# Kernel optimization log

Measured on AMD Instinct MI355X. Metric: run time of the kernel, lower is better.

Reference implementation:

```python
import jax, jax.numpy as jnp
import numpy as np

N = 50000      # num_nodes
F_IN = 128     # num_features
E = 800000     # num edges (before self-loops)
H1, D1 = 8, 16 # conv1: 8 heads x 16 dims -> 128 concat
D2 = 8         # conv2: 1 head x 8 dims
NEG_SLOPE = 0.2


def setup_inputs() -> dict:
    key = jax.random.key(0)
    ks = jax.random.split(key, 16)
    s = 0.05
    return {
        "x": jax.random.normal(ks[0], (N, F_IN), jnp.float32),
        "edge_index": jax.random.randint(ks[1], (2, E), 0, N, dtype=jnp.int64),
        "W1": jax.random.normal(ks[2], (F_IN, H1 * D1), jnp.float32) * s,
        "att_src1": jax.random.normal(ks[3], (H1, D1), jnp.float32) * s,
        "att_dst1": jax.random.normal(ks[4], (H1, D1), jnp.float32) * s,
        "b1": jnp.zeros((H1 * D1,), jnp.float32),
        "W2": jax.random.normal(ks[5], (H1 * D1, D2), jnp.float32) * s,
        "att_src2": jax.random.normal(ks[6], (1, D2), jnp.float32) * s,
        "att_dst2": jax.random.normal(ks[7], (1, D2), jnp.float32) * s,
        "b2": jnp.zeros((D2,), jnp.float32),
        "fc1_w": jax.random.normal(ks[8], (N * D2, 84), jnp.float32) * 0.005,
        "fc1_b": jnp.zeros((84,), jnp.float32),
        "fc2_w": jax.random.normal(ks[9], (84, 24), jnp.float32) * s,
        "fc2_b": jnp.zeros((24,), jnp.float32),
        "fc3_w": jax.random.normal(ks[10], (24, 2), jnp.float32) * s,
        "fc3_b": jnp.zeros((2,), jnp.float32),
    }


def gat_conv(x, src, dst, W, att_src, att_dst, bias, heads, out_dim):
    """PyG GATConv: per-head linear, edge attention, scatter-softmax over
    incoming edges per target node, weighted scatter-add aggregation."""
    n = x.shape[0]
    h = (x @ W).reshape(n, heads, out_dim)            # [N,H,D]
    a_src = jnp.einsum('nhd,hd->nh', h, att_src)      # [N,H]
    a_dst = jnp.einsum('nhd,hd->nh', h, att_dst)      # [N,H]
    e = jax.nn.leaky_relu(a_src[src] + a_dst[dst], NEG_SLOPE)  # [Et,H]
    # softmax over edges grouped by destination node (stable)
    m = jax.ops.segment_max(e, dst, num_segments=n)
    p = jnp.exp(e - m[dst])
    denom = jax.ops.segment_sum(p, dst, num_segments=n)
    alpha = p / denom[dst]                            # [Et,H]
    out = jax.ops.segment_sum(alpha[:, :, None] * h[src], dst, num_segments=n)
    return out.reshape(n, heads * out_dim) + bias


def reference(x, edge_index, W1, att_src1, att_dst1, b1,
              W2, att_src2, att_dst2, b2,
              fc1_w, fc1_b, fc2_w, fc2_b, fc3_w, fc3_b):
    # add self-loops (GATConv default add_self_loops=True)
    loop = jnp.arange(N, dtype=edge_index.dtype)
    src = jnp.concatenate([edge_index[0], loop])
    dst = jnp.concatenate([edge_index[1], loop])

    h = jax.nn.elu(gat_conv(x, src, dst, W1, att_src1, att_dst1, b1, H1, D1))
    h = jax.nn.elu(gat_conv(h, src, dst, W2, att_src2, att_dst2, b2, 1, D2))

    z = h.reshape(1, N * D2)                          # batch of one graph
    z = jax.nn.elu(z @ fc1_w + fc1_b)
    z = jax.nn.elu(z @ fc2_w + fc2_b)
    z = z @ fc3_w + fc3_b
    return jax.nn.log_softmax(z, axis=1)              # [1,2]
```

## Files before the change

### kernel.cpp

```cpp
#include <hip/hip_runtime.h>
#include <math.h>

#define N_NODES 50000
#define F_IN 128
#define NE 800000
#define NH1 8
#define ND1 16
#define ND2 8
#define NEG 0.2f
#define ZLEN (N_NODES * ND2)

typedef __attribute__((ext_vector_type(8))) short bf16x8;
typedef __attribute__((ext_vector_type(4))) float f32x4;

__device__ __forceinline__ float lrelu(float v) { return v > 0.f ? v : NEG * v; }
__device__ __forceinline__ float elu1(float v)  { return v > 0.f ? v : (__expf(v) - 1.f); }

__device__ __forceinline__ unsigned short f2bf(float f) {
    union { float f; unsigned int i; } c; c.f = f;
    unsigned int u = c.i;
    return (unsigned short)((u + 0x7FFFu + ((u >> 16) & 1u)) >> 16);
}
__device__ __forceinline__ float bflo(unsigned int u) {
    union { unsigned int i; float f; } c; c.i = u << 16; return c.f;
}
__device__ __forceinline__ float bfhi(unsigned int u) {
    union { unsigned int i; float f; } c; c.i = u & 0xFFFF0000u; return c.f;
}
__device__ __forceinline__ int ei_is64(const int* __restrict__ ei) {
    return ((ei[1] | ei[3] | ei[5] | ei[7]) == 0) ? 1 : 0;
}

__global__ void init_counts_kernel(int* __restrict__ counts) {
    int i = blockIdx.x * blockDim.x + threadIdx.x;
    if (i < N_NODES) counts[i] = 1;
}

__global__ void hist_kernel(const int* __restrict__ ei, int* __restrict__ counts) {
    int e = blockIdx.x * blockDim.x + threadIdx.x;
    if (e >= NE) return;
    int is64 = ei_is64(ei);
    int d = is64 ? ei[2 * NE + 2 * e] : ei[NE + e];
    atomicAdd(&counts[d], 1);
}

__global__ __launch_bounds__(1024) void scan_kernel(const int* __restrict__ counts,
                                                    int* __restrict__ rowptr,
                                                    int* __restrict__ cursor) {
    __shared__ int wsum[16];
    __shared__ int wpre[16];
    __shared__ int s_total;
    const int t = threadIdx.x;
    const int lane = t & 63, w = t >> 6;
    int carry = 0;
    if (t == 0) rowptr[0] = 0;
    for (int base = 0; base < N_NODES; base += 1024) {
        int i = base + t;
        int orig = (i < N_NODES) ? counts[i] : 0;
        int v = orig;
        #pragma unroll
        for (int off = 1; off < 64; off <<= 1) {
            int u = __shfl_up(v, off, 64);
            if (lane >= off) v += u;
        }
        if (lane == 63) wsum[w] = v;
        __syncthreads();
        if (t == 0) {
            int s = 0;
            #pragma unroll
            for (int j = 0; j < 16; ++j) { wpre[j] = s; s += wsum[j]; }
            s_total = s;
        }
        __syncthreads();
        int incl = v + wpre[w] + carry;
        if (i < N_NODES) { rowptr[i + 1] = incl; cursor[i] = incl - orig; }
        carry += s_total;
        __syncthreads();
    }
}

__global__ void fill_kernel(const int* __restrict__ ei,
                            int* __restrict__ cursor, int* __restrict__ esrc) {
    int i = blockIdx.x * blockDim.x + threadIdx.x;
    if (i >= NE + N_NODES) return;
    int s, d;
    if (i < NE) {
        int is64 = ei_is64(ei);
        if (is64) { s = ei[2 * i]; d = ei[2 * NE + 2 * i]; }
        else      { s = ei[i];     d = ei[NE + i]; }
    } else {
        s = d = i - NE;
    }
    int slot = atomicAdd(&cursor[d], 1);
    esrc[slot] = s;
}

__global__ __launch_bounds__(256) void wprep_kernel(const float* __restrict__ W,
                                                    uint4* __restrict__ wbf) {
    int tid = blockIdx.x * 256 + threadIdx.x;
    int col = tid >> 4, kc = tid & 15;
    unsigned int u[4];
    #pragma unroll
    for (int jj = 0; jj < 4; ++jj) {
        unsigned int lo = f2bf(W[(kc * 8 + 2 * jj) * 128 + col]);
        unsigned int hi = f2bf(W[(kc * 8 + 2 * jj + 1) * 128 + col]);
        u[jj] = lo | (hi << 16);
    }
    uint4 v; v.x = u[0]; v.y = u[1]; v.z = u[2]; v.w = u[3];
    wbf[col * 16 + (kc ^ (col & 15))] = v;
}

__global__ __launch_bounds__(256) void gemm1_kernel(const float* __restrict__ x,
                                                    const uint4* __restrict__ wbf,
                                                    const float* __restrict__ att_src,
                                                    const float* __restrict__ att_dst,
                                                    unsigned int* __restrict__ h1b,
                                                    float* __restrict__ a_src1,
                                                    float* __restrict__ a_dst1) {
    __shared__ uint4 Xs[1024];
    __shared__ uint4 Ws[2048];
    const int t = threadIdx.x;
    const int row0 = blockIdx.x * 64;

    #pragma unroll
    for (int p = 0; p < 8; ++p) Ws[p * 256 + t] = wbf[p * 256 + t];

    #pragma unroll
    for (int p = 0; p < 4; ++p) {
        int cidx = p * 256 + t;
        int row = cidx >> 4, c = cidx & 15;
        int grow = row0 + row;
        float4 xa = make_float4(0.f, 0.f, 0.f, 0.f);
        float4 xb = make_float4(0.f, 0.f, 0.f, 0.f);
        if (grow < N_NODES) {
            xa = *reinterpret_cast<const float4*>(x + (size_t)grow * F_IN + c * 8);
            xb = *reinterpret_cast<const float4*>(x + (size_t)grow * F_IN + c * 8 + 4);
        }
        uint4 u;
        u.x = (unsigned int)f2bf(xa.x) | ((unsigned int)f2bf(xa.y) << 16);
        u.y = (unsigned int)f2bf(xa.z) | ((unsigned int)f2bf(xa.w) << 16);
        u.z = (unsigned int)f2bf(xb.x) | ((unsigned int)f2bf(xb.y) << 16);
        u.w = (unsigned int)f2bf(xb.z) | ((unsigned int)f2bf(xb.w) << 16);
        Xs[row * 16 + (c ^ (row & 15))] = u;
    }
    __syncthreads();

    const int wv = t >> 6;
    const int l  = t & 63;
    const int d  = l & 15;
    const int g  = l >> 4;
    const int arow = wv * 16 + d;

    f32x4 acc[8];
    #pragma unroll
    for (int n = 0; n < 8; ++n) { acc[n][0] = 0.f; acc[n][1] = 0.f; acc[n][2] = 0.f; acc[n][3] = 0.f; }

    #pragma unroll
    for (int ks = 0; ks < 4; ++ks) {
        int kc = ks * 4 + g;
        union { uint4 u; bf16x8 v; } A;
        A.u = Xs[arow * 16 + (kc ^ d)];
        #pragma unroll
        for (int n = 0; n < 8; ++n) {
            union { uint4 u; bf16x8 v; } B;
            B.u = Ws[(n * 16 + d) * 16 + (kc ^ d)];
            acc[n] = __builtin_amdgcn_mfma_f32_16x16x32_bf16(A.v, B.v, acc[n], 0, 0, 0);
        }
    }

    float as8[8], ad8[8];
    #pragma unroll
    for (int n = 0; n < 8; ++n) { as8[n] = att_src[n * 16 + d]; ad8[n] = att_dst[n * 16 + d]; }
    #pragma unroll
    for (int n = 0; n < 8; ++n) {
        #pragma unroll
        for (int r = 0; r < 4; ++r) {
            float ps = acc[n][r] * as8[n];
            float pd = acc[n][r] * ad8[n];
            #pragma unroll
            for (int off = 1; off < 16; off <<= 1) {
                ps += __shfl_xor(ps, off, 16);
                pd += __shfl_xor(pd, off, 16);
            }
            int grow = row0 + wv * 16 + g * 4 + r;
            if (d == 0 && grow < N_NODES) {
                a_src1[grow * 8 + n] = ps;
                a_dst1[grow * 8 + n] = pd;
            }
        }
    }
    #pragma unroll
    for (int n = 0; n < 8; ++n) {
        #pragma unroll
        for (int r = 0; r < 4; ++r) {
            float lo = acc[n][r];
            float hi = __shfl_xor(lo, 1, 64);
            int grow = row0 + wv * 16 + g * 4 + r;
            if (((d & 1) == 0) && grow < N_NODES) {
                unsigned int u = (unsigned int)f2bf(lo) | ((unsigned int)f2bf(hi) << 16);
                h1b[(size_t)grow * 64 + n * 8 + (d >> 1)] = u;
            }
        }
    }
}

__global__ __launch_bounds__(256) void agg1_kernel(const unsigned int* __restrict__ h1b,
                                                   const float* __restrict__ a_src,
                                                   const float* __restrict__ a_dst,
                                                   const int* __restrict__ rowptr,
                                                   const int* __restrict__ esrc,
                                                   const float* __restrict__ b1,
                                                   float* __restrict__ hout) {
    int wid = (blockIdx.x * 256 + threadIdx.x) >> 6;
    if (wid >= N_NODES) return;
    const int lane = threadIdx.x & 63;
    const int h = lane >> 3;
    const float ad = a_dst[wid * 8 + h];
    float acc0 = 0.f, acc1 = 0.f, den = 0.f;
    int j = rowptr[wid];
    const int jend = rowptr[wid + 1];
    for (; j + 4 <= jend; j += 4) {
        int s0 = esrc[j], s1 = esrc[j + 1], s2 = esrc[j + 2], s3 = esrc[j + 3];
        float e0 = a_src[s0 * 8 + h], e1 = a_src[s1 * 8 + h];
        float e2 = a_src[s2 * 8 + h], e3 = a_src[s3 * 8 + h];
        unsigned int u0 = h1b[(size_t)s0 * 64 + lane];
        unsigned int u1 = h1b[(size_t)s1 * 64 + lane];
        unsigned int u2 = h1b[(size_t)s2 * 64 + lane];
        unsigned int u3 = h1b[(size_t)s3 * 64 + lane];
        float p0 = __expf(lrelu(e0 + ad));
        float p1 = __expf(lrelu(e1 + ad));
        float p2 = __expf(lrelu(e2 + ad));
        float p3 = __expf(lrelu(e3 + ad));
        den += (p0 + p1) + (p2 + p3);
        acc0 = fmaf(p0, bflo(u0), acc0); acc1 = fmaf(p0, bfhi(u0), acc1);
        acc0 = fmaf(p1, bflo(u1), acc0); acc1 = fmaf(p1, bfhi(u1), acc1);
        acc0 = fmaf(p2, bflo(u2), acc0); acc1 = fmaf(p2, bfhi(u2), acc1);
        acc0 = fmaf(p3, bflo(u3), acc0); acc1 = fmaf(p3, bfhi(u3), acc1);
    }
    for (; j < jend; ++j) {
        int s = esrc[j];
        float e = a_src[s * 8 + h];
        unsigned int u = h1b[(size_t)s * 64 + lane];
        float p = __expf(lrelu(e + ad));
        den += p;
        acc0 = fmaf(p, bflo(u), acc0);
        acc1 = fmaf(p, bfhi(u), acc1);
    }
    float inv = 1.f / den;
    float2 bb = *reinterpret_cast<const float2*>(b1 + 2 * lane);
    float o0 = elu1(acc0 * inv + bb.x);
    float o1 = elu1(acc1 * inv + bb.y);
    *reinterpret_cast<float2*>(hout + (size_t)wid * F_IN + 2 * lane) = make_float2(o0, o1);
}

__global__ __launch_bounds__(256) void gemm2_kernel(const float* __restrict__ h,
                                                    const float* __restrict__ W2,
                                                    const float* __restrict__ att_src2,
                                                    const float* __restrict__ att_dst2,
                                                    float* __restrict__ h2,
                                                    float* __restrict__ a_src2,
                                                    float* __restrict__ a_dst2) {
    __shared__ float Ws[F_IN * ND2];
    __shared__ float Hs[32 * 132];
    int t = threadIdx.x;
    int node0 = blockIdx.x * 32;
    #pragma unroll
    for (int i = 0; i < 4; ++i) { int idx = i * 256 + t; Ws[idx] = W2[idx]; }
    #pragma unroll
    for (int i = 0; i < 4; ++i) {
        int fidx = i * 256 + t;
        int r = fidx >> 5;
        int c4 = fidx & 31;
        int grow = node0 + r;
        float4 v = make_float4(0.f, 0.f, 0.f, 0.f);
        if (grow < N_NODES) v = *reinterpret_cast<const float4*>(h + (size_t)grow * F_IN + c4 * 4);
        *reinterpret_cast<float4*>(&Hs[r * 132 + c4 * 4]) = v;
    }
    __syncthreads();
    int nsub = t >> 3, d = t & 7;
    int node = node0 + nsub;
    float acc = 0.f;
    #pragma unroll 8
    for (int k = 0; k < F_IN; ++k)
        acc = fmaf(Hs[nsub * 132 + k], Ws[k * ND2 + d], acc);
    float vs = acc * att_src2[d];
    float vd = acc * att_dst2[d];
    #pragma unroll
    for (int off = 4; off >= 1; off >>= 1) {
        vs += __shfl_xor(vs, off, 8);
        vd += __shfl_xor(vd, off, 8);
    }
    if (node < N_NODES) {
        h2[node * ND2 + d] = acc;
        if (d == 0) { a_src2[node] = vs; a_dst2[node] = vd; }
    }
}

__global__ __launch_bounds__(256) void agg2fc1_kernel(const float* __restrict__ h2,
                                                      const float* __restrict__ a_src2,
                                                      const float* __restrict__ a_dst2,
                                                      const int* __restrict__ rowptr,
                                                      const int* __restrict__ esrc,
                                                      const float* __restrict__ b2,
                                                      const float* __restrict__ w,
                                                      float* __restrict__ partial) {
    __shared__ float zs[2048];
    __shared__ float4 red[252];
    const int t = threadIdx.x;
    const int n = blockIdx.x * 256 + t;

    float z[8] = {0.f, 0.f, 0.f, 0.f, 0.f, 0.f, 0.f, 0.f};
    if (n < N_NODES) {
        float ad = a_dst2[n];
        float den = 0.f;
        const int jend = rowptr[n + 1];
        for (int j = rowptr[n]; j < jend; ++j) {
            int s = esrc[j];
            float p = __expf(lrelu(a_src2[s] + ad));
            den += p;
            float4 va = *reinterpret_cast<const float4*>(h2 + s * ND2);
            float4 vb = *reinterpret_cast<const float4*>(h2 + s * ND2 + 4);
            z[0] = fmaf(p, va.x, z[0]); z[1] = fmaf(p, va.y, z[1]);
            z[2] = fmaf(p, va.z, z[2]); z[3] = fmaf(p, va.w, z[3]);
            z[4] = fmaf(p, vb.x, z[4]); z[5] = fmaf(p, vb.y, z[5]);
            z[6] = fmaf(p, vb.z, z[6]); z[7] = fmaf(p, vb.w, z[7]);
        }
        float inv = 1.f / den;
        #pragma unroll
        for (int k = 0; k < 8; ++k) z[k] = elu1(z[k] * inv + b2[k]);
    }
    *reinterpret_cast<float4*>(&zs[t * 8])     = make_float4(z[0], z[1], z[2], z[3]);
    *reinterpret_cast<float4*>(&zs[t * 8 + 4]) = make_float4(z[4], z[5], z[6], z[7]);
    __syncthreads();

    const int c4 = t % 21;
    const int rr = t / 21;
    if (t < 252) {
        float4 a = make_float4(0.f, 0.f, 0.f, 0.f);
        const float4* __restrict__ w4 = reinterpret_cast<const float4*>(w);
        const size_t R0 = (size_t)blockIdx.x * 2048;
        if (R0 + 2048 <= (size_t)ZLEN) {
            for (int gq = 0; gq < 34; ++gq) {
                float4 wv[5];
                float  zv[5];
                #pragma unroll
                for (int u = 0; u < 5; ++u) {
                    int i = (gq * 5 + u) * 12 + rr;
                    wv[u] = w4[(R0 + i) * 21 + c4];
                    zv[u] = zs[i];
                }
                #pragma unroll
                for (int u = 0; u < 5; ++u) {
                    a.x = fmaf(zv[u], wv[u].x, a.x);
                    a.y = fmaf(zv[u], wv[u].y, a.y);
                    a.z = fmaf(zv[u], wv[u].z, a.z);
                    a.w = fmaf(zv[u], wv[u].w, a.w);
                }
            }
            if (rr < 8) {
                int i = 2040 + rr;
                float4 wv = w4[(R0 + i) * 21 + c4];
                float  zv = zs[i];
                a.x = fmaf(zv, wv.x, a.x); a.y = fmaf(zv, wv.y, a.y);
                a.z = fmaf(zv, wv.z, a.z); a.w = fmaf(zv, wv.w, a.w);
            }
        } else {
            for (int i = rr; i < 2048; i += 12) {
                if (R0 + i < (size_t)ZLEN) {
                    float4 wv = w4[(R0 + i) * 21 + c4];
                    float  zv = zs[i];
                    a.x = fmaf(zv, wv.x, a.x); a.y = fmaf(zv, wv.y, a.y);
                    a.z = fmaf(zv, wv.z, a.z); a.w = fmaf(zv, wv.w, a.w);
                }
            }
        }
        red[t] = a;
    }
    __syncthreads();
    if (t < 21) {
        float4 s = red[t];
        #pragma unroll
        for (int k = 1; k < 12; ++k) {
            float4 v = red[k * 21 + t];
            s.x += v.x; s.y += v.y; s.z += v.z; s.w += v.w;
        }
        *reinterpret_cast<float4*>(partial + (size_t)blockIdx.x * 88 + t * 4) = s;
    }
}

__global__ __launch_bounds__(256) void fctail_kernel(const float* __restrict__ partial,
                                                     const float* __restrict__ fc1_b,
                                                     const float* __restrict__ fc2_w,
                                                     const float* __restrict__ fc2_b,
                                                     const float* __restrict__ fc3_w,
                                                     const float* __restrict__ fc3_b,
                                                     float* __restrict__ out) {
    __shared__ float red[252];
    __shared__ float z1[84];
    __shared__ float z2[24];
    const int t = threadIdx.x;
    if (t < 252) {
        const int j = t % 84;
        const int sl = t / 84;
        const int b0 = sl * 66;
        const int b1 = (b0 + 66 < 196) ? (b0 + 66) : 196;
        float s = 0.f;
        for (int b = b0; b < b1; b += 2)
            s += partial[(size_t)b * 88 + j] + partial[(size_t)(b + 1) * 88 + j];
        red[t] = s;
    }
    __syncthreads();
    if (t < 84) z1[t] = elu1(red[t] + red[t + 84] + red[t + 168] + fc1_b[t]);
    __syncthreads();
    if (t < 24) {
        float a = fc2_b[t];
        for (int i = 0; i < 84; ++i) a = fmaf(z1[i], fc2_w[i * 24 + t], a);
        z2[t] = elu1(a);
    }
    __syncthreads();
    if (t == 0) {
        float z3[2];
        #pragma unroll
        for (int jj = 0; jj < 2; ++jj) {
            float a = fc3_b[jj];
            for (int i = 0; i < 24; ++i) a = fmaf(z2[i], fc3_w[i * 2 + jj], a);
            z3[jj] = a;
        }
        float m = fmaxf(z3[0], z3[1]);
        float l = m + logf(__expf(z3[0] - m) + __expf(z3[1] - m));
        out[0] = z3[0] - l;
        out[1] = z3[1] - l;
    }
}

extern "C" void kernel_launch(void* const* d_in, const int* in_sizes, int n_in,
                              void* d_out, int out_size, void* d_ws, size_t ws_size,
                              hipStream_t stream) {
    const float* x        = (const float*)d_in[0];
    const int*   ei       = (const int*)d_in[1];
    const float* W1       = (const float*)d_in[2];
    const float* att_src1 = (const float*)d_in[3];
    const float* att_dst1 = (const float*)d_in[4];
    const float* b1       = (const float*)d_in[5];
    const float* W2       = (const float*)d_in[6];
    const float* att_src2 = (const float*)d_in[7];
    const float* att_dst2 = (const float*)d_in[8];
    const float* b2       = (const float*)d_in[9];
    const float* fc1_w    = (const float*)d_in[10];
    const float* fc1_b    = (const float*)d_in[11];
    const float* fc2_w    = (const float*)d_in[12];
    const float* fc2_b    = (const float*)d_in[13];
    const float* fc3_w    = (const float*)d_in[14];
    const float* fc3_b    = (const float*)d_in[15];
    float* out = (float*)d_out;

    char* ws = (char*)d_ws;
    unsigned int* h1b = (unsigned int*)(ws + 0);
    float* hbuf   = (float*)(ws + 12800000);
    float* a_src1 = (float*)(ws + 38400000);
    float* a_dst1 = (float*)(ws + 40000000);
    float* h2     = (float*)(ws + 41600000);
    float* a_src2 = (float*)(ws + 43200000);
    float* a_dst2 = (float*)(ws + 43400000);
    int*   counts = (int*)  (ws + 43600000);
    int*   rowptr = (int*)  (ws + 43800000);
    int*   cursor = (int*)  (ws + 44000064);
    int*   esrc   = (int*)  (ws + 44200064);
    float* partial= (float*)(ws + 47600064);
    uint4* wbf    = (uint4*)(ws + 47669056);

    wprep_kernel<<<8, 256, 0, stream>>>(W1, wbf);
    init_counts_kernel<<<(N_NODES + 255) / 256, 256, 0, stream>>>(counts);
    hist_kernel<<<(NE + 255) / 256, 256, 0, stream>>>(ei, counts);
    scan_kernel<<<1, 1024, 0, stream>>>(counts, rowptr, cursor);
    fill_kernel<<<(NE + N_NODES + 255) / 256, 256, 0, stream>>>(ei, cursor, esrc);

    gemm1_kernel<<<(N_NODES + 63) / 64, 256, 0, stream>>>(x, wbf, att_src1, att_dst1, h1b, a_src1, a_dst1);
    agg1_kernel<<<(N_NODES + 3) / 4, 256, 0, stream>>>(h1b, a_src1, a_dst1, rowptr, esrc, b1, hbuf);

    gemm2_kernel<<<(N_NODES + 31) / 32, 256, 0, stream>>>(hbuf, W2, att_src2, att_dst2, h2, a_src2, a_dst2);
    agg2fc1_kernel<<<(N_NODES + 255) / 256, 256, 0, stream>>>(h2, a_src2, a_dst2, rowptr, esrc, b2, fc1_w, partial);
    fctail_kernel<<<1, 256, 0, stream>>>(partial, fc1_b, fc2_w, fc2_b, fc3_w, fc3_b, out);
}
```

Measured before the change: 273.9 us.

## Parallelize scan, split agg2 from FC1, widen FC1 grid, unroll agg1 by eight

The single-block serial scan is replaced by a three-kernel multi-block scan. The fused agg2+fc1 kernel is split into a standalone agg2 kernel that writes node features to a buffer, followed by an fc1 stage launched with many more blocks (240 rows each), so streaming the 134MB fc1 weight uses the whole GPU rather than 196 blocks. wprep and init_counts are merged into one prep kernel, and agg1 gains an 8-wide unrolled gather loop for more memory-level parallelism. The cost is extra launches, an intermediate buffer round trip and a larger final reduction over partial sums.

```diff
diff --git a/kernel.cpp b/kernel.cpp
--- a/kernel.cpp
+++ b/kernel.cpp
@@ -9,6 +9,9 @@
 #define ND2 8
 #define NEG 0.2f
 #define ZLEN (N_NODES * ND2)
+#define NBLK 196
+#define FC1_RPB 240
+#define FC1_NB 1667
 
 typedef __attribute__((ext_vector_type(8))) short bf16x8;
 typedef __attribute__((ext_vector_type(4))) float f32x4;
@@ -31,9 +34,23 @@
     return ((ei[1] | ei[3] | ei[5] | ei[7]) == 0) ? 1 : 0;
 }
 
-__global__ void init_counts_kernel(int* __restrict__ counts) {
-    int i = blockIdx.x * blockDim.x + threadIdx.x;
+__global__ __launch_bounds__(256) void prep_kernel(const float* __restrict__ W,
+                                                   uint4* __restrict__ wbf,
+                                                   int* __restrict__ counts) {
+    int i = blockIdx.x * 256 + threadIdx.x;
     if (i < N_NODES) counts[i] = 1;
+    if (i < 2048) {
+        int col = i >> 4, kc = i & 15;
+        unsigned int u[4];
+        #pragma unroll
+        for (int jj = 0; jj < 4; ++jj) {
+            unsigned int lo = f2bf(W[(kc * 8 + 2 * jj) * 128 + col]);
+            unsigned int hi = f2bf(W[(kc * 8 + 2 * jj + 1) * 128 + col]);
+            u[jj] = lo | (hi << 16);
+        }
+        uint4 v; v.x = u[0]; v.y = u[1]; v.z = u[2]; v.w = u[3];
+        wbf[col * 16 + (kc ^ (col & 15))] = v;
+    }
 }
 
 __global__ void hist_kernel(const int* __restrict__ ei, int* __restrict__ counts) {
@@ -44,39 +61,62 @@
     atomicAdd(&counts[d], 1);
 }
 
-__global__ __launch_bounds__(1024) void scan_kernel(const int* __restrict__ counts,
+__global__ __launch_bounds__(256) void scan1_kernel(const int* __restrict__ counts,
+                                                    int* __restrict__ bsum) {
+    const int t = threadIdx.x;
+    int i = blockIdx.x * 256 + t;
+    int v = (i < N_NODES) ? counts[i] : 0;
+    #pragma unroll
+    for (int off = 32; off; off >>= 1) v += __shfl_down(v, off, 64);
+    __shared__ int ws[4];
+    if ((t & 63) == 0) ws[t >> 6] = v;
+    __syncthreads();
+    if (t == 0) bsum[blockIdx.x] = ws[0] + ws[1] + ws[2] + ws[3];
+}
+
+__global__ __launch_bounds__(256) void scan2_kernel(const int* __restrict__ bsum,
+                                                    int* __restrict__ boff) {
+    const int t = threadIdx.x;
+    const int lane = t & 63, w = t >> 6;
+    int v = (t < NBLK) ? bsum[t] : 0;
+    int incl = v;
+    #pragma unroll
+    for (int off = 1; off < 64; off <<= 1) {
+        int u = __shfl_up(incl, off, 64);
+        if (lane >= off) incl += u;
+    }
+    __shared__ int wsum[4];
+    __shared__ int wpre[4];
+    if (lane == 63) wsum[w] = incl;
+    __syncthreads();
+    if (t == 0) { int s = 0; for (int j = 0; j < 4; ++j) { wpre[j] = s; s += wsum[j]; } }
+    __syncthreads();
+    if (t < NBLK) boff[t] = incl - v + wpre[w];
+}
+
+__global__ __launch_bounds__(256) void scan3_kernel(const int* __restrict__ counts,
+                                                    const int* __restrict__ boff,
                                                     int* __restrict__ rowptr,
                                                     int* __restrict__ cursor) {
-    __shared__ int wsum[16];
-    __shared__ int wpre[16];
-    __shared__ int s_total;
     const int t = threadIdx.x;
     const int lane = t & 63, w = t >> 6;
-    int carry = 0;
-    if (t == 0) rowptr[0] = 0;
-    for (int base = 0; base < N_NODES; base += 1024) {
-        int i = base + t;
-        int orig = (i < N_NODES) ? counts[i] : 0;
-        int v = orig;
-        #pragma unroll
-        for (int off = 1; off < 64; off <<= 1) {
-            int u = __shfl_up(v, off, 64);
-            if (lane >= off) v += u;
-        }
-        if (lane == 63) wsum[w] = v;
-        __syncthreads();
-        if (t == 0) {
-            int s = 0;
-            #pragma unroll
-            for (int j = 0; j < 16; ++j) { wpre[j] = s; s += wsum[j]; }
-            s_total = s;
-        }
-        __syncthreads();
-        int incl = v + wpre[w] + carry;
-        if (i < N_NODES) { rowptr[i + 1] = incl; cursor[i] = incl - orig; }
-        carry += s_total;
-        __syncthreads();
-    }
+    int i = blockIdx.x * 256 + t;
+    int v = (i < N_NODES) ? counts[i] : 0;
+    int incl = v;
+    #pragma unroll
+    for (int off = 1; off < 64; off <<= 1) {
+        int u = __shfl_up(incl, off, 64);
+        if (lane >= off) incl += u;
+    }
+    __shared__ int wsum[4];
+    __shared__ int wpre[4];
+    if (lane == 63) wsum[w] = incl;
+    __syncthreads();
+    if (t == 0) { int s = 0; for (int j = 0; j < 4; ++j) { wpre[j] = s; s += wsum[j]; } }
+    __syncthreads();
+    incl += wpre[w] + boff[blockIdx.x];
+    if (i < N_NODES) { rowptr[i + 1] = incl; cursor[i] = incl - v; }
+    if (i == 0) rowptr[0] = 0;
 }
 
 __global__ void fill_kernel(const int* __restrict__ ei,
@@ -93,21 +133,6 @@
     }
     int slot = atomicAdd(&cursor[d], 1);
     esrc[slot] = s;
-}
-
-__global__ __launch_bounds__(256) void wprep_kernel(const float* __restrict__ W,
-                                                    uint4* __restrict__ wbf) {
-    int tid = blockIdx.x * 256 + threadIdx.x;
-    int col = tid >> 4, kc = tid & 15;
-    unsigned int u[4];
-    #pragma unroll
-    for (int jj = 0; jj < 4; ++jj) {
-        unsigned int lo = f2bf(W[(kc * 8 + 2 * jj) * 128 + col]);
-        unsigned int hi = f2bf(W[(kc * 8 + 2 * jj + 1) * 128 + col]);
-        u[jj] = lo | (hi << 16);
-    }
-    uint4 v; v.x = u[0]; v.y = u[1]; v.z = u[2]; v.w = u[3];
-    wbf[col * 16 + (kc ^ (col & 15))] = v;
 }
 
 __global__ __launch_bounds__(256) void gemm1_kernel(const float* __restrict__ x,
@@ -219,14 +244,32 @@
     float acc0 = 0.f, acc1 = 0.f, den = 0.f;
     int j = rowptr[wid];
     const int jend = rowptr[wid + 1];
+    for (; j + 8 <= jend; j += 8) {
+        int s[8];
+        #pragma unroll
+        for (int k = 0; k < 8; ++k) s[k] = esrc[j + k];
+        unsigned int u[8];
+        #pragma unroll
+        for (int k = 0; k < 8; ++k) u[k] = h1b[(size_t)s[k] * 64 + lane];
+        float e[8];
+        #pragma unroll
+        for (int k = 0; k < 8; ++k) e[k] = a_src[s[k] * 8 + h];
+        #pragma unroll
+        for (int k = 0; k < 8; ++k) {
+            float p = __expf(lrelu(e[k] + ad));
+            den += p;
+            acc0 = fmaf(p, bflo(u[k]), acc0);
+            acc1 = fmaf(p, bfhi(u[k]), acc1);
+        }
+    }
     for (; j + 4 <= jend; j += 4) {
         int s0 = esrc[j], s1 = esrc[j + 1], s2 = esrc[j + 2], s3 = esrc[j + 3];
-        float e0 = a_src[s0 * 8 + h], e1 = a_src[s1 * 8 + h];
-        float e2 = a_src[s2 * 8 + h], e3 = a_src[s3 * 8 + h];
         unsigned int u0 = h1b[(size_t)s0 * 64 + lane];
         unsigned int u1 = h1b[(size_t)s1 * 64 + lane];
         unsigned int u2 = h1b[(size_t)s2 * 64 + lane];
         unsigned int u3 = h1b[(size_t)s3 * 64 + lane];
+        float e0 = a_src[s0 * 8 + h], e1 = a_src[s1 * 8 + h];
+        float e2 = a_src[s2 * 8 + h], e3 = a_src[s3 * 8 + h];
         float p0 = __expf(lrelu(e0 + ad));
         float p1 = __expf(lrelu(e1 + ad));
         float p2 = __expf(lrelu(e2 + ad));
@@ -239,8 +282,8 @@
     }
     for (; j < jend; ++j) {
         int s = esrc[j];
+        unsigned int u = h1b[(size_t)s * 64 + lane];
         float e = a_src[s * 8 + h];
-        unsigned int u = h1b[(size_t)s * 64 + lane];
         float p = __expf(lrelu(e + ad));
         den += p;
         acc0 = fmaf(p, bflo(u), acc0);
@@ -296,78 +339,77 @@
     }
 }
 
-__global__ __launch_bounds__(256) void agg2fc1_kernel(const float* __restrict__ h2,
-                                                      const float* __restrict__ a_src2,
-                                                      const float* __restrict__ a_dst2,
-                                                      const int* __restrict__ rowptr,
-                                                      const int* __restrict__ esrc,
-                                                      const float* __restrict__ b2,
-                                                      const float* __restrict__ w,
-                                                      float* __restrict__ partial) {
-    __shared__ float zs[2048];
+__global__ void agg2_kernel(const float* __restrict__ h2,
+                            const float* __restrict__ a_src2, const float* __restrict__ a_dst2,
+                            const int* __restrict__ rowptr, const int* __restrict__ esrc,
+                            const float* __restrict__ b2, float* __restrict__ g) {
+    int n = blockIdx.x * blockDim.x + threadIdx.x;
+    if (n >= N_NODES) return;
+    float ad = a_dst2[n];
+    float acc[8] = {0.f, 0.f, 0.f, 0.f, 0.f, 0.f, 0.f, 0.f};
+    float den = 0.f;
+    int jend = rowptr[n + 1];
+    for (int j = rowptr[n]; j < jend; ++j) {
+        int s = esrc[j];
+        float p = __expf(lrelu(a_src2[s] + ad));
+        den += p;
+        float4 va = *reinterpret_cast<const float4*>(h2 + s * ND2);
+        float4 vb = *reinterpret_cast<const float4*>(h2 + s * ND2 + 4);
+        acc[0] = fmaf(p, va.x, acc[0]); acc[1] = fmaf(p, va.y, acc[1]);
+        acc[2] = fmaf(p, va.z, acc[2]); acc[3] = fmaf(p, va.w, acc[3]);
+        acc[4] = fmaf(p, vb.x, acc[4]); acc[5] = fmaf(p, vb.y, acc[5]);
+        acc[6] = fmaf(p, vb.z, acc[6]); acc[7] = fmaf(p, vb.w, acc[7]);
+    }
+    float inv = 1.f / den;
+    float4 o0 = make_float4(elu1(acc[0] * inv + b2[0]), elu1(acc[1] * inv + b2[1]),
+                            elu1(acc[2] * inv + b2[2]), elu1(acc[3] * inv + b2[3]));
+    float4 o1 = make_float4(elu1(acc[4] * inv + b2[4]), elu1(acc[5] * inv + b2[5]),
+                            elu1(acc[6] * inv + b2[6]), elu1(acc[7] * inv + b2[7]));
+    *reinterpret_cast<float4*>(g + n * ND2)     = o0;
+    *reinterpret_cast<float4*>(g + n * ND2 + 4) = o1;
+}
+
+__global__ __launch_bounds__(256) void fc1_stage1(const float* __restrict__ z,
+                                                  const float* __restrict__ w,
+                                                  float* __restrict__ partial) {
+    __shared__ float zs[FC1_RPB];
     __shared__ float4 red[252];
     const int t = threadIdx.x;
-    const int n = blockIdx.x * 256 + t;
-
-    float z[8] = {0.f, 0.f, 0.f, 0.f, 0.f, 0.f, 0.f, 0.f};
-    if (n < N_NODES) {
-        float ad = a_dst2[n];
-        float den = 0.f;
-        const int jend = rowptr[n + 1];
-        for (int j = rowptr[n]; j < jend; ++j) {
-            int s = esrc[j];
-            float p = __expf(lrelu(a_src2[s] + ad));
-            den += p;
-            float4 va = *reinterpret_cast<const float4*>(h2 + s * ND2);
-            float4 vb = *reinterpret_cast<const float4*>(h2 + s * ND2 + 4);
-            z[0] = fmaf(p, va.x, z[0]); z[1] = fmaf(p, va.y, z[1]);
-            z[2] = fmaf(p, va.z, z[2]); z[3] = fmaf(p, va.w, z[3]);
-            z[4] = fmaf(p, vb.x, z[4]); z[5] = fmaf(p, vb.y, z[5]);
-            z[6] = fmaf(p, vb.z, z[6]); z[7] = fmaf(p, vb.w, z[7]);
-        }
-        float inv = 1.f / den;
-        #pragma unroll
-        for (int k = 0; k < 8; ++k) z[k] = elu1(z[k] * inv + b2[k]);
-    }
-    *reinterpret_cast<float4*>(&zs[t * 8])     = make_float4(z[0], z[1], z[2], z[3]);
-    *reinterpret_cast<float4*>(&zs[t * 8 + 4]) = make_float4(z[4], z[5], z[6], z[7]);
-    __syncthreads();
-
+    const int b = blockIdx.x;
+    const int r0 = b * FC1_RPB;
+    if (t < FC1_RPB) {
+        int gr = r0 + t;
+        zs[t] = (gr < ZLEN) ? z[gr] : 0.f;
+    }
+    __syncthreads();
     const int c4 = t % 21;
     const int rr = t / 21;
     if (t < 252) {
         float4 a = make_float4(0.f, 0.f, 0.f, 0.f);
         const float4* __restrict__ w4 = reinterpret_cast<const float4*>(w);
-        const size_t R0 = (size_t)blockIdx.x * 2048;
-        if (R0 + 2048 <= (size_t)ZLEN) {
-            for (int gq = 0; gq < 34; ++gq) {
-                float4 wv[5];
-                float  zv[5];
+        if (r0 + FC1_RPB <= ZLEN) {
+            #pragma unroll
+            for (int bq = 0; bq < 5; ++bq) {
+                float4 wv[4];
+                float  zv[4];
                 #pragma unroll
-                for (int u = 0; u < 5; ++u) {
-                    int i = (gq * 5 + u) * 12 + rr;
-                    wv[u] = w4[(R0 + i) * 21 + c4];
+                for (int u = 0; u < 4; ++u) {
+                    int i = bq * 48 + u * 12 + rr;
+                    wv[u] = w4[(size_t)(r0 + i) * 21 + c4];
                     zv[u] = zs[i];
                 }
                 #pragma unroll
-                for (int u = 0; u < 5; ++u) {
+                for (int u = 0; u < 4; ++u) {
                     a.x = fmaf(zv[u], wv[u].x, a.x);
                     a.y = fmaf(zv[u], wv[u].y, a.y);
                     a.z = fmaf(zv[u], wv[u].z, a.z);
                     a.w = fmaf(zv[u], wv[u].w, a.w);
                 }
             }
-            if (rr < 8) {
-                int i = 2040 + rr;
-                float4 wv = w4[(R0 + i) * 21 + c4];
-                float  zv = zs[i];
-                a.x = fmaf(zv, wv.x, a.x); a.y = fmaf(zv, wv.y, a.y);
-                a.z = fmaf(zv, wv.z, a.z); a.w = fmaf(zv, wv.w, a.w);
-            }
         } else {
-            for (int i = rr; i < 2048; i += 12) {
-                if (R0 + i < (size_t)ZLEN) {
-                    float4 wv = w4[(R0 + i) * 21 + c4];
+            for (int i = rr; i < FC1_RPB; i += 12) {
+                if (r0 + i < ZLEN) {
+                    float4 wv = w4[(size_t)(r0 + i) * 21 + c4];
                     float  zv = zs[i];
                     a.x = fmaf(zv, wv.x, a.x); a.y = fmaf(zv, wv.y, a.y);
                     a.z = fmaf(zv, wv.z, a.z); a.w = fmaf(zv, wv.w, a.w);
@@ -384,33 +426,36 @@
             float4 v = red[k * 21 + t];
             s.x += v.x; s.y += v.y; s.z += v.z; s.w += v.w;
         }
-        *reinterpret_cast<float4*>(partial + (size_t)blockIdx.x * 88 + t * 4) = s;
-    }
-}
-
-__global__ __launch_bounds__(256) void fctail_kernel(const float* __restrict__ partial,
-                                                     const float* __restrict__ fc1_b,
-                                                     const float* __restrict__ fc2_w,
-                                                     const float* __restrict__ fc2_b,
-                                                     const float* __restrict__ fc3_w,
-                                                     const float* __restrict__ fc3_b,
-                                                     float* __restrict__ out) {
-    __shared__ float red[252];
+        *reinterpret_cast<float4*>(partial + (size_t)b * 88 + t * 4) = s;
+    }
+}
+
+__global__ __launch_bounds__(1024) void fctail_kernel(const float* __restrict__ partial,
+                                                      const float* __restrict__ fc1_b,
+                                                      const float* __restrict__ fc2_w,
+                                                      const float* __restrict__ fc2_b,
+                                                      const float* __restrict__ fc3_w,
+                                                      const float* __restrict__ fc3_b,
+                                                      float* __restrict__ out) {
+    __shared__ float red[1008];
     __shared__ float z1[84];
     __shared__ float z2[24];
     const int t = threadIdx.x;
-    if (t < 252) {
-        const int j = t % 84;
+    if (t < 1008) {
+        const int j  = t % 84;
         const int sl = t / 84;
-        const int b0 = sl * 66;
-        const int b1 = (b0 + 66 < 196) ? (b0 + 66) : 196;
         float s = 0.f;
-        for (int b = b0; b < b1; b += 2)
-            s += partial[(size_t)b * 88 + j] + partial[(size_t)(b + 1) * 88 + j];
+        for (int b = sl; b < FC1_NB; b += 12)
+            s += partial[(size_t)b * 88 + j];
         red[t] = s;
     }
     __syncthreads();
-    if (t < 84) z1[t] = elu1(red[t] + red[t + 84] + red[t + 168] + fc1_b[t]);
+    if (t < 84) {
+        float s = 0.f;
+        #pragma unroll
+        for (int sl = 0; sl < 12; ++sl) s += red[sl * 84 + t];
+        z1[t] = elu1(s + fc1_b[t]);
+    }
     __syncthreads();
     if (t < 24) {
         float a = fc2_b[t];
@@ -462,23 +507,29 @@
     float* h2     = (float*)(ws + 41600000);
     float* a_src2 = (float*)(ws + 43200000);
     float* a_dst2 = (float*)(ws + 43400000);
-    int*   counts = (int*)  (ws + 43600000);
-    int*   rowptr = (int*)  (ws + 43800000);
-    int*   cursor = (int*)  (ws + 44000064);
-    int*   esrc   = (int*)  (ws + 44200064);
-    float* partial= (float*)(ws + 47600064);
-    uint4* wbf    = (uint4*)(ws + 47669056);
-
-    wprep_kernel<<<8, 256, 0, stream>>>(W1, wbf);
-    init_counts_kernel<<<(N_NODES + 255) / 256, 256, 0, stream>>>(counts);
+    float* g      = (float*)(ws + 43600000);
+    int*   counts = (int*)  (ws + 45200000);
+    int*   rowptr = (int*)  (ws + 45400000);
+    int*   cursor = (int*)  (ws + 45600064);
+    int*   esrc   = (int*)  (ws + 45800064);
+    float* partial= (float*)(ws + 49200064);
+    uint4* wbf    = (uint4*)(ws + 49786848);
+    int*   bsum   = (int*)  (ws + 49819616);
+    int*   boff   = (int*)  (ws + 49820400);
+
+    prep_kernel<<<NBLK, 256, 0, stream>>>(W1, wbf, counts);
     hist_kernel<<<(NE + 255) / 256, 256, 0, stream>>>(ei, counts);
-    scan_kernel<<<1, 1024, 0, stream>>>(counts, rowptr, cursor);
+    scan1_kernel<<<NBLK, 256, 0, stream>>>(counts, bsum);
+    scan2_kernel<<<1, 256, 0, stream>>>(bsum, boff);
+    scan3_kernel<<<NBLK, 256, 0, stream>>>(counts, boff, rowptr, cursor);
     fill_kernel<<<(NE + N_NODES + 255) / 256, 256, 0, stream>>>(ei, cursor, esrc);
 
     gemm1_kernel<<<(N_NODES + 63) / 64, 256, 0, stream>>>(x, wbf, att_src1, att_dst1, h1b, a_src1, a_dst1);
     agg1_kernel<<<(N_NODES + 3) / 4, 256, 0, stream>>>(h1b, a_src1, a_dst1, rowptr, esrc, b1, hbuf);
 
     gemm2_kernel<<<(N_NODES + 31) / 32, 256, 0, stream>>>(hbuf, W2, att_src2, att_dst2, h2, a_src2, a_dst2);
-    agg2fc1_kernel<<<(N_NODES + 255) / 256, 256, 0, stream>>>(h2, a_src2, a_dst2, rowptr, esrc, b2, fc1_w, partial);
-    fctail_kernel<<<1, 256, 0, stream>>>(partial, fc1_b, fc2_w, fc2_b, fc3_w, fc3_b, out);
-}
+    agg2_kernel<<<(N_NODES + 255) / 256, 256, 0, stream>>>(h2, a_src2, a_dst2, rowptr, esrc, b2, g);
+
+    fc1_stage1<<<FC1_NB, 256, 0, stream>>>(g, fc1_w, partial);
+    fctail_kernel<<<1, 1024, 0, stream>>>(partial, fc1_b, fc2_w, fc2_b, fc3_w, fc3_b, out);
+}
```

Result: faster. 256.5 us (-6.4%).
